# Optimization experiments

Measured on AMD Instinct MI355X. Metric: run time of the kernel, lower is better.

Reference implementation:

```python
import jax, jax.numpy as jnp
import numpy as np

N = 100000      # num nodes
E = 1600000     # num edges (avg degree 16)
D_IN = 64
D_OUT = 32
NEG_SLOPE = 0.01  # torch LeakyReLU default


def setup_inputs() -> dict:
    key = jax.random.key(0)
    k1, k2, k3, k4 = jax.random.split(key, 4)
    x = jax.random.normal(k1, (N, D_IN), dtype=jnp.float32)
    edge_index = jax.random.randint(k2, (2, E), 0, N, dtype=jnp.int32)
    # GCNConv linear weights (glorot-ish init) and biases
    W1 = jax.random.normal(k3, (D_IN, D_IN), dtype=jnp.float32) / np.float32(np.sqrt(D_IN))
    b1 = jnp.zeros((D_IN,), dtype=jnp.float32)
    W2 = jax.random.normal(k4, (D_IN, D_OUT), dtype=jnp.float32) / np.float32(np.sqrt(D_IN))
    b2 = jnp.zeros((D_OUT,), dtype=jnp.float32)
    return {"x": x, "edge_index": edge_index, "W1": W1, "b1": b1, "W2": W2, "b2": b2}


def reference(x, edge_index, W1, b1, W2, b2):
    # PyG GCNConv default: add self-loops, symmetric normalization D^-1/2 (A+I) D^-1/2
    loops = jnp.arange(N, dtype=edge_index.dtype)
    src = jnp.concatenate([edge_index[0], loops])  # [E+N]
    dst = jnp.concatenate([edge_index[1], loops])  # [E+N]
    deg = jax.ops.segment_sum(jnp.ones(src.shape[0], jnp.float32), dst, num_segments=N)
    dinv = jax.lax.rsqrt(deg)  # deg >= 1 due to self-loops
    norm = dinv[src] * dinv[dst]  # [E+N]

    def gcn_conv(h, W, b):
        h = h @ W                          # [N, d_out]
        msg = h[src] * norm[:, None]       # gather + normalize  [E+N, d_out]
        return jax.ops.segment_sum(msg, dst, num_segments=N) + b  # scatter-add

    h = gcn_conv(x, W1, b1)
    h = jnp.where(h > 0, h, NEG_SLOPE * h)  # LeakyReLU
    return gcn_conv(h, W2, b2)
```

## Files before the change

kernel.cpp:

```cpp
#include <hip/hip_runtime.h>

#define N_NODES 100000
#define N_EDGES 1600000
#define DIN 64
#define DOUT 32
#define NEG_SLOPE 0.01f
#define NBUCK 196
#define CAP 12288
#define CH 4096
#define NB1 ((N_EDGES + CH - 1) / CH)

__device__ inline unsigned short f2bf(float f) {
    unsigned int u = __float_as_uint(f);
    unsigned int r = (u + 0x7fffu + ((u >> 16) & 1u)) >> 16;
    return (unsigned short)r;
}
__device__ inline float bflo(unsigned int p) { return __uint_as_float(p << 16); }
__device__ inline float bfhi(unsigned int p) { return __uint_as_float(p & 0xffff0000u); }
#define NTL(p) __builtin_nontemporal_load(p)

__device__ inline void addpack4(float* a, uint4 r) {
    a[0] += bflo(r.x); a[1] += bfhi(r.x);
    a[2] += bflo(r.y); a[3] += bfhi(r.y);
    a[4] += bflo(r.z); a[5] += bfhi(r.z);
    a[6] += bflo(r.w); a[7] += bfhi(r.w);
}
__device__ inline void addpack2(float* a, uint2 r) {
    a[0] += bflo(r.x); a[1] += bfhi(r.x);
    a[2] += bflo(r.y); a[3] += bfhi(r.y);
}

__global__ void zero_bf_kernel(int* __restrict__ bucketfill) {
    if (threadIdx.x < NBUCK) bucketfill[threadIdx.x] = 0;
}

__global__ __launch_bounds__(256) void binpass1_kernel(const int* __restrict__ src,
                                                       const int* __restrict__ dst,
                                                       int* __restrict__ bucketfill,
                                                       unsigned int* __restrict__ staging2) {
    __shared__ int hist[NBUCK];
    __shared__ int base[NBUCK];
    __shared__ int gbase[NBUCK];
    __shared__ int scanbuf[256];
    __shared__ unsigned int sorted[CH];
    int tid = threadIdx.x;
    int b = blockIdx.x;
    for (int t = tid; t < NBUCK; t += 256) hist[t] = 0;
    __syncthreads();

    int e0 = b * CH + tid;
    int bk[16];
    int rk[16];
    unsigned int pay[16];
#pragma unroll
    for (int i = 0; i < 16; ++i) {
        int e = e0 + i * 256;
        if (e < N_EDGES) {
            int d = NTL(&dst[e]);
            int s = NTL(&src[e]);
            bk[i] = d >> 9;
            pay[i] = (unsigned int)s | ((unsigned int)(d & 511) << 17);
            rk[i] = atomicAdd(&hist[bk[i]], 1);
        } else {
            bk[i] = -1;
        }
    }
    __syncthreads();
    int v = (tid < NBUCK) ? hist[tid] : 0;
    scanbuf[tid] = v;
    __syncthreads();
    for (int off = 1; off < 256; off <<= 1) {
        int a = scanbuf[tid];
        int add = (tid >= off) ? scanbuf[tid - off] : 0;
        __syncthreads();
        scanbuf[tid] = a + add;
        __syncthreads();
    }
    if (tid < NBUCK) {
        base[tid] = scanbuf[tid] - v;
        gbase[tid] = v ? atomicAdd(&bucketfill[tid], v) : 0;
    }
    __syncthreads();
#pragma unroll
    for (int i = 0; i < 16; ++i) {
        if (bk[i] >= 0) sorted[base[bk[i]] + rk[i]] = pay[i];
    }
    __syncthreads();
    int wv = tid >> 6, ln = tid & 63;
    for (int k = wv; k < NBUCK; k += 4) {
        int h = hist[k];
        int b0 = base[k];
        int g0 = gbase[k];
        unsigned int* dp = staging2 + (size_t)k * CAP;
        for (int i = ln; i < h; i += 64)
            if (g0 + i < CAP) dp[g0 + i] = sorted[b0 + i];
    }
}

__global__ __launch_bounds__(1024) void binpass2_kernel(const unsigned int* __restrict__ staging2,
                                                        const int* __restrict__ bucketfill,
                                                        int* __restrict__ rowptr,
                                                        float* __restrict__ dinv,
                                                        int* __restrict__ colsrc) {
    __shared__ int hist[512];
    __shared__ int posl[512];
    __shared__ int sh[512];
    __shared__ int red[4];
    int k = blockIdx.x;
    int tid = threadIdx.x;
    int base_node = k << 9;
    int nn = min(512, N_NODES - base_node);
    int len = min(bucketfill[k], CAP);

    if (tid < 256) {
        int v = (tid < k) ? bucketfill[tid] : 0;
#pragma unroll
        for (int off = 32; off; off >>= 1) v += __shfl_down(v, off);
        if ((tid & 63) == 0) red[tid >> 6] = v;
    }
    if (tid < 512) hist[tid] = 0;
    __syncthreads();
    int bbase = red[0] + red[1] + red[2] + red[3];
    const unsigned int* stg = staging2 + (size_t)k * CAP;

    for (int i = tid; i < len; i += 1024) atomicAdd(&hist[stg[i] >> 17], 1);
    __syncthreads();

    int v = 0;
    if (tid < 512) { v = hist[tid]; sh[tid] = v; }
    __syncthreads();
    for (int off = 1; off < 512; off <<= 1) {
        int a = 0, add = 0;
        if (tid < 512) { a = sh[tid]; add = (tid >= off) ? sh[tid - off] : 0; }
        __syncthreads();
        if (tid < 512) sh[tid] = a + add;
        __syncthreads();
    }
    if (tid < 512) {
        int excl = sh[tid] - v;
        posl[tid] = bbase + excl;
        if (tid < nn) {
            rowptr[base_node + tid] = bbase + excl;
            dinv[base_node + tid] = rsqrtf((float)(v + 1));
        }
    }
    if (k == NBUCK - 1 && tid == 0) rowptr[N_NODES] = N_EDGES;
    __syncthreads();
    for (int i = tid; i < len; i += 1024) {
        unsigned int pay = stg[i];
        int idx = atomicAdd(&posl[pay >> 17], 1);
        colsrc[idx] = (int)(pay & 0x1FFFFu);
    }
}

__global__ __launch_bounds__(256) void gemm_k64_n64_kernel(const float* __restrict__ X,
                                                           const float* __restrict__ W,
                                                           const float* __restrict__ dinv,
                                                           unsigned short* __restrict__ Hn) {
    __shared__ float Ws[64 * 64];
    __shared__ float Xs[64][65];
    int tid = threadIdx.x;
    int row0 = blockIdx.x * 64;
    {
        const float4* Wv = (const float4*)W;
        float4* Wsv = (float4*)Ws;
#pragma unroll
        for (int i = 0; i < 4; ++i) Wsv[tid + 256 * i] = Wv[tid + 256 * i];
    }
#pragma unroll
    for (int i = 0; i < 4; ++i) {
        int s = tid + i * 256;
        int r = s >> 4, c = (s & 15) * 4;
        int gr = row0 + r;
        float4 xv = (gr < N_NODES) ? *(const float4*)(X + (size_t)gr * 64 + c)
                                   : make_float4(0.f, 0.f, 0.f, 0.f);
        Xs[r][c] = xv.x; Xs[r][c + 1] = xv.y; Xs[r][c + 2] = xv.z; Xs[r][c + 3] = xv.w;
    }
    __syncthreads();

    int c4 = (tid & 15) * 4;
    int r4 = (tid >> 4) * 4;
    float a0[4] = {}, a1[4] = {}, a2[4] = {}, a3[4] = {};
#pragma unroll 8
    for (int k = 0; k < 64; ++k) {
        float4 w = *(const float4*)&Ws[(k << 6) + c4];
        float x0 = Xs[r4][k], x1 = Xs[r4 + 1][k], x2 = Xs[r4 + 2][k], x3 = Xs[r4 + 3][k];
        a0[0] += x0 * w.x; a0[1] += x0 * w.y; a0[2] += x0 * w.z; a0[3] += x0 * w.w;
        a1[0] += x1 * w.x; a1[1] += x1 * w.y; a1[2] += x1 * w.z; a1[3] += x1 * w.w;
        a2[0] += x2 * w.x; a2[1] += x2 * w.y; a2[2] += x2 * w.z; a2[3] += x2 * w.w;
        a3[0] += x3 * w.x; a3[1] += x3 * w.y; a3[2] += x3 * w.z; a3[3] += x3 * w.w;
    }
    float* accs[4] = {a0, a1, a2, a3};
#pragma unroll
    for (int r = 0; r < 4; ++r) {
        int gr = row0 + r4 + r;
        if (gr < N_NODES) {
            float dv = dinv[gr];
            float* a = accs[r];
            unsigned int lo = (unsigned int)f2bf(a[0] * dv) | ((unsigned int)f2bf(a[1] * dv) << 16);
            unsigned int hi = (unsigned int)f2bf(a[2] * dv) | ((unsigned int)f2bf(a[3] * dv) << 16);
            *(uint2*)(Hn + (size_t)gr * 64 + c4) = make_uint2(lo, hi);
        }
    }
}

__global__ void gemm_k64_n32_bf16_kernel(const unsigned short* __restrict__ Xb,
                                         const float* __restrict__ W,
                                         const float* __restrict__ dinv,
                                         unsigned short* __restrict__ Hn) {
    __shared__ float Ws[64 * 32];
    __shared__ float Xs[8][64];
    int tid = threadIdx.x;
    {
        const float4* Wv = (const float4*)W;
        float4* Wsv = (float4*)Ws;
#pragma unroll
        for (int i = 0; i < 2; ++i) Wsv[tid + 256 * i] = Wv[tid + 256 * i];
    }
    int row0 = blockIdx.x * 8;
    {
        unsigned int w = ((const unsigned int*)(Xb + (size_t)row0 * 64))[tid];
        int r = tid >> 5, p = (tid & 31) << 1;
        Xs[r][p] = bflo(w);
        Xs[r][p + 1] = bfhi(w);
    }
    __syncthreads();

    int r = tid >> 5;
    int col = tid & 31;
    float sum = 0.f;
#pragma unroll
    for (int k = 0; k < 64; ++k) sum += Xs[r][k] * Ws[k * 32 + col];
    Hn[(size_t)(row0 + r) * 32 + col] = f2bf(sum * dinv[row0 + r]);
}

__global__ __launch_bounds__(256) void gather64_kernel(
    const unsigned short* __restrict__ Hn, const int* __restrict__ rowptr,
    const int* __restrict__ colsrc, const float* __restrict__ dinv,
    const float* __restrict__ bias, unsigned short* __restrict__ h1b) {
    int gwid = (blockIdx.x * blockDim.x + threadIdx.x) >> 6;
    int lane = threadIdx.x & 63;
    int g = lane >> 3, sl = lane & 7, gb = g << 3;
    int v = gwid * 8 + g;
    if (v >= N_NODES) return;
    int beg = rowptr[v], end = rowptr[v + 1];

    float acc[8], ac2[8];
#pragma unroll
    for (int i = 0; i < 8; ++i) { acc[i] = 0.f; ac2[i] = 0.f; }
    {
        uint4 rw = ((const uint4*)(Hn + (size_t)v * 64))[sl];
        addpack4(acc, rw);
    }
    for (int t0 = beg; t0 < end; t0 += 8) {
        int sv = (t0 + sl < end) ? colsrc[t0 + sl] : 0;
        int cnt = min(8, end - t0);
        int t = 0;
        for (; t + 2 <= cnt; t += 2) {
            int s0 = __shfl(sv, gb + t);
            int s1 = __shfl(sv, gb + t + 1);
            uint4 r0 = ((const uint4*)(Hn + (size_t)s0 * 64))[sl];
            uint4 r1 = ((const uint4*)(Hn + (size_t)s1 * 64))[sl];
            addpack4(acc, r0);
            addpack4(ac2, r1);
        }
        if (t < cnt) {
            int s0 = __shfl(sv, gb + t);
            uint4 r0 = ((const uint4*)(Hn + (size_t)s0 * 64))[sl];
            addpack4(acc, r0);
        }
    }
    float dv = dinv[v];
    float4 b0 = ((const float4*)(bias + sl * 8))[0];
    float4 b1v = ((const float4*)(bias + sl * 8))[1];
    float o[8];
    o[0] = (acc[0] + ac2[0]) * dv + b0.x;  o[1] = (acc[1] + ac2[1]) * dv + b0.y;
    o[2] = (acc[2] + ac2[2]) * dv + b0.z;  o[3] = (acc[3] + ac2[3]) * dv + b0.w;
    o[4] = (acc[4] + ac2[4]) * dv + b1v.x; o[5] = (acc[5] + ac2[5]) * dv + b1v.y;
    o[6] = (acc[6] + ac2[6]) * dv + b1v.z; o[7] = (acc[7] + ac2[7]) * dv + b1v.w;
#pragma unroll
    for (int i = 0; i < 8; ++i) o[i] = o[i] > 0.f ? o[i] : NEG_SLOPE * o[i];
    uint4 pk;
    pk.x = (unsigned int)f2bf(o[0]) | ((unsigned int)f2bf(o[1]) << 16);
    pk.y = (unsigned int)f2bf(o[2]) | ((unsigned int)f2bf(o[3]) << 16);
    pk.z = (unsigned int)f2bf(o[4]) | ((unsigned int)f2bf(o[5]) << 16);
    pk.w = (unsigned int)f2bf(o[6]) | ((unsigned int)f2bf(o[7]) << 16);
    *(uint4*)(h1b + (size_t)v * 64 + sl * 8) = pk;
}

__global__ __launch_bounds__(256) void gather32_kernel(
    const unsigned short* __restrict__ Hn, const int* __restrict__ rowptr,
    const int* __restrict__ colsrc, const float* __restrict__ dinv,
    const float* __restrict__ bias, float* __restrict__ out) {
    int gwid = (blockIdx.x * blockDim.x + threadIdx.x) >> 6;
    int lane = threadIdx.x & 63;
    int g = lane >> 3, sl = lane & 7, gb = g << 3;
    int v = gwid * 8 + g;
    if (v >= N_NODES) return;
    int beg = rowptr[v], end = rowptr[v + 1];

    float acc[4], ac2[4];
#pragma unroll
    for (int i = 0; i < 4; ++i) { acc[i] = 0.f; ac2[i] = 0.f; }
    {
        uint2 rw = ((const uint2*)(Hn + (size_t)v * 32))[sl];
        addpack2(acc, rw);
    }
    for (int t0 = beg; t0 < end; t0 += 8) {
        int sv = (t0 + sl < end) ? colsrc[t0 + sl] : 0;
        int cnt = min(8, end - t0);
        int t = 0;
        for (; t + 2 <= cnt; t += 2) {
            int s0 = __shfl(sv, gb + t);
            int s1 = __shfl(sv, gb + t + 1);
            uint2 r0 = ((const uint2*)(Hn + (size_t)s0 * 32))[sl];
            uint2 r1 = ((const uint2*)(Hn + (size_t)s1 * 32))[sl];
            addpack2(acc, r0);
            addpack2(ac2, r1);
        }
        if (t < cnt) {
            int s0 = __shfl(sv, gb + t);
            uint2 r0 = ((const uint2*)(Hn + (size_t)s0 * 32))[sl];
            addpack2(acc, r0);
        }
    }
    float dv = dinv[v];
    float4 bb = ((const float4*)bias)[sl];
    float o0 = (acc[0] + ac2[0]) * dv + bb.x;
    float o1 = (acc[1] + ac2[1]) * dv + bb.y;
    float o2 = (acc[2] + ac2[2]) * dv + bb.z;
    float o3 = (acc[3] + ac2[3]) * dv + bb.w;
    *(float4*)(out + (size_t)v * 32 + sl * 4) = make_float4(o0, o1, o2, o3);
}

extern "C" void kernel_launch(void* const* d_in, const int* in_sizes, int n_in,
                              void* d_out, int out_size, void* d_ws, size_t ws_size,
                              hipStream_t stream) {
    const float* x = (const float*)d_in[0];
    const int* ei = (const int*)d_in[1];
    const float* W1 = (const float*)d_in[2];
    const float* b1 = (const float*)d_in[3];
    const float* W2 = (const float*)d_in[4];
    const float* b2 = (const float*)d_in[5];
    float* out = (float*)d_out;

    const int* src = ei;
    const int* dst = ei + N_EDGES;

    char* p = (char*)d_ws;
    auto alloc = [&](size_t bytes) { char* r = p; p += (bytes + 255) & ~(size_t)255; return r; };
    float* dinv = (float*)alloc(N_NODES * 4);
    int* rowptr = (int*)alloc((N_NODES + 1) * 4);
    int* bucketfill = (int*)alloc(NBUCK * 4);
    int* colsrc = (int*)alloc((size_t)N_EDGES * 4);
    unsigned short* h1n = (unsigned short*)alloc((size_t)N_NODES * DIN * 2);
    unsigned short* h1b = (unsigned short*)alloc((size_t)N_NODES * DIN * 2);
    unsigned short* h2n = (unsigned short*)alloc((size_t)N_NODES * DOUT * 2);
    unsigned int* staging2 = (unsigned int*)alloc((size_t)NBUCK * CAP * 4);

    zero_bf_kernel<<<1, 256, 0, stream>>>(bucketfill);
    binpass1_kernel<<<NB1, 256, 0, stream>>>(src, dst, bucketfill, staging2);
    binpass2_kernel<<<NBUCK, 1024, 0, stream>>>(staging2, bucketfill, rowptr, dinv, colsrc);

    gemm_k64_n64_kernel<<<(N_NODES + 63) / 64, 256, 0, stream>>>(x, W1, dinv, h1n);

    gather64_kernel<<<(N_NODES / 8 * 64) / 256, 256, 0, stream>>>(
        h1n, rowptr, colsrc, dinv, b1, h1b);

    gemm_k64_n32_bf16_kernel<<<N_NODES / 8, 256, 0, stream>>>(h1b, W2, dinv, h2n);

    gather32_kernel<<<(N_NODES / 8 * 64) / 256, 256, 0, stream>>>(
        h2n, rowptr, colsrc, dinv, b2, out);
}
```

Measured before the change: 147.8 us.

## Per-wave LDS histograms in binning, batched 8-way gather loads, memset for bucketfill

The binning pass now keeps one shared-memory histogram per wave to cut LDS atomic contention, then prefix-sums the per-wave counts to place each edge. Both gather kernels issue all eight neighbour-row loads of a full chunk before accumulating, which raises memory-level parallelism at the cost of more registers; partial chunks keep the old path. The one-thread zeroing kernel is replaced by hipMemsetAsync.

```diff
diff --git a/kernel.cpp b/kernel.cpp
--- a/kernel.cpp
+++ b/kernel.cpp
@@ -30,22 +30,20 @@
     a[2] += bflo(r.y); a[3] += bfhi(r.y);
 }
 
-__global__ void zero_bf_kernel(int* __restrict__ bucketfill) {
-    if (threadIdx.x < NBUCK) bucketfill[threadIdx.x] = 0;
-}
-
 __global__ __launch_bounds__(256) void binpass1_kernel(const int* __restrict__ src,
                                                        const int* __restrict__ dst,
                                                        int* __restrict__ bucketfill,
                                                        unsigned int* __restrict__ staging2) {
-    __shared__ int hist[NBUCK];
+    __shared__ int histw[4][NBUCK];
     __shared__ int base[NBUCK];
+    __shared__ int tot[NBUCK];
     __shared__ int gbase[NBUCK];
     __shared__ int scanbuf[256];
     __shared__ unsigned int sorted[CH];
     int tid = threadIdx.x;
+    int w = tid >> 6;
     int b = blockIdx.x;
-    for (int t = tid; t < NBUCK; t += 256) hist[t] = 0;
+    for (int t = tid; t < 4 * NBUCK; t += 256) ((int*)histw)[t] = 0;
     __syncthreads();
 
     int e0 = b * CH + tid;
@@ -60,14 +58,23 @@
             int s = NTL(&src[e]);
             bk[i] = d >> 9;
             pay[i] = (unsigned int)s | ((unsigned int)(d & 511) << 17);
-            rk[i] = atomicAdd(&hist[bk[i]], 1);
+            rk[i] = atomicAdd(&histw[w][bk[i]], 1);
         } else {
             bk[i] = -1;
         }
     }
     __syncthreads();
-    int v = (tid < NBUCK) ? hist[tid] : 0;
-    scanbuf[tid] = v;
+    int v = 0;
+    if (tid < NBUCK) {
+        int h0 = histw[0][tid], h1 = histw[1][tid], h2 = histw[2][tid], h3 = histw[3][tid];
+        histw[0][tid] = 0;
+        histw[1][tid] = h0;
+        histw[2][tid] = h0 + h1;
+        histw[3][tid] = h0 + h1 + h2;
+        v = h0 + h1 + h2 + h3;
+        tot[tid] = v;
+    }
+    scanbuf[tid] = (tid < NBUCK) ? v : 0;
     __syncthreads();
     for (int off = 1; off < 256; off <<= 1) {
         int a = scanbuf[tid];
@@ -83,12 +90,12 @@
     __syncthreads();
 #pragma unroll
     for (int i = 0; i < 16; ++i) {
-        if (bk[i] >= 0) sorted[base[bk[i]] + rk[i]] = pay[i];
+        if (bk[i] >= 0) sorted[base[bk[i]] + histw[w][bk[i]] + rk[i]] = pay[i];
     }
     __syncthreads();
     int wv = tid >> 6, ln = tid & 63;
     for (int k = wv; k < NBUCK; k += 4) {
-        int h = hist[k];
+        int h = tot[k];
         int b0 = base[k];
         int g0 = gbase[k];
         unsigned int* dp = staging2 + (size_t)k * CAP;
@@ -252,9 +259,24 @@
         uint4 rw = ((const uint4*)(Hn + (size_t)v * 64))[sl];
         addpack4(acc, rw);
     }
-    for (int t0 = beg; t0 < end; t0 += 8) {
+    int t0 = beg;
+    for (; t0 + 8 <= end; t0 += 8) {
+        int sv = colsrc[t0 + sl];
+        uint4 r[8];
+#pragma unroll
+        for (int t = 0; t < 8; ++t) {
+            int s = __shfl(sv, gb + t);
+            r[t] = ((const uint4*)(Hn + (size_t)s * 64))[sl];
+        }
+#pragma unroll
+        for (int t = 0; t < 8; t += 2) {
+            addpack4(acc, r[t]);
+            addpack4(ac2, r[t + 1]);
+        }
+    }
+    if (t0 < end) {
         int sv = (t0 + sl < end) ? colsrc[t0 + sl] : 0;
-        int cnt = min(8, end - t0);
+        int cnt = end - t0;
         int t = 0;
         for (; t + 2 <= cnt; t += 2) {
             int s0 = __shfl(sv, gb + t);
@@ -306,9 +328,24 @@
         uint2 rw = ((const uint2*)(Hn + (size_t)v * 32))[sl];
         addpack2(acc, rw);
     }
-    for (int t0 = beg; t0 < end; t0 += 8) {
+    int t0 = beg;
+    for (; t0 + 8 <= end; t0 += 8) {
+        int sv = colsrc[t0 + sl];
+        uint2 r[8];
+#pragma unroll
+        for (int t = 0; t < 8; ++t) {
+            int s = __shfl(sv, gb + t);
+            r[t] = ((const uint2*)(Hn + (size_t)s * 32))[sl];
+        }
+#pragma unroll
+        for (int t = 0; t < 8; t += 2) {
+            addpack2(acc, r[t]);
+            addpack2(ac2, r[t + 1]);
+        }
+    }
+    if (t0 < end) {
         int sv = (t0 + sl < end) ? colsrc[t0 + sl] : 0;
-        int cnt = min(8, end - t0);
+        int cnt = end - t0;
         int t = 0;
         for (; t + 2 <= cnt; t += 2) {
             int s0 = __shfl(sv, gb + t);
@@ -358,7 +395,7 @@
     unsigned short* h2n = (unsigned short*)alloc((size_t)N_NODES * DOUT * 2);
     unsigned int* staging2 = (unsigned int*)alloc((size_t)NBUCK * CAP * 4);
 
-    zero_bf_kernel<<<1, 256, 0, stream>>>(bucketfill);
+    hipMemsetAsync(bucketfill, 0, NBUCK * sizeof(int), stream);
     binpass1_kernel<<<NB1, 256, 0, stream>>>(src, dst, bucketfill, staging2);
     binpass2_kernel<<<NBUCK, 1024, 0, stream>>>(staging2, bucketfill, rowptr, dinv, colsrc);
 
```

Result: faster. 143.9 us (-2.6%).
